# Performance work log

Measured on AMD Instinct MI355X. Metric: run time of the kernel, lower is better.

The kernel has to match this reference:

```python
import jax, jax.numpy as jnp
import numpy as np

L, D, H, S, V, B = 8, 512, 8, 64, 66, 256
DH = D // H
EPS = 1e-10  # module's LayerNorm eps, added to std (not var)


def layernorm(x, g, b):
    # torch.std_mean default: unbiased std (ddof=1)
    mean = jnp.mean(x, axis=-1, keepdims=True)
    std = jnp.std(x, axis=-1, ddof=1, keepdims=True)
    return (x - mean) / (std + EPS) * g + b


def setup_inputs() -> dict:
    key = jax.random.key(0)
    ks = iter(jax.random.split(key, 32))
    def n(shape, scale=0.02):
        return jax.random.normal(next(ks), shape, dtype=jnp.float32) * scale
    return {
        "input_ids": jax.random.randint(next(ks), (B, S), 0, V),
        "targets": jax.random.randint(next(ks), (B, S), 0, V),
        "tok_emb": n((V, D), 1.0),
        "pos_emb": n((S, D), 1.0),
        "Wq": n((L, D, H, DH)), "Wk": n((L, D, H, DH)), "Wv": n((L, D, H, DH)),
        "Wo": n((L, D, D)), "bo": jnp.zeros((L, D), jnp.float32),
        "W1": n((L, D, 4 * D)), "b1": jnp.zeros((L, 4 * D), jnp.float32),
        "W2": n((L, 4 * D, D)), "b2": jnp.zeros((L, D), jnp.float32),
        "ln1_g": jnp.ones((L, D), jnp.float32), "ln1_b": jnp.zeros((L, D), jnp.float32),
        "ln2_g": jnp.ones((L, D), jnp.float32), "ln2_b": jnp.zeros((L, D), jnp.float32),
        "lnf_g": jnp.ones((D,), jnp.float32), "lnf_b": jnp.zeros((D,), jnp.float32),
        "Wu": n((D, V)), "bu": jnp.zeros((V,), jnp.float32),
    }


def reference(input_ids, targets, tok_emb, pos_emb, Wq, Wk, Wv, Wo, bo,
              W1, b1, W2, b2, ln1_g, ln1_b, ln2_g, ln2_b, lnf_g, lnf_b, Wu, bu):
    x = tok_emb[input_ids] + pos_emb[None, :, :]  # [B,S,D]
    scale = 1.0 / jnp.sqrt(jnp.float32(D))        # module scales by 1/sqrt(d_model)
    mask = jnp.tril(jnp.ones((S, S), dtype=bool))
    for l in range(L):
        h = layernorm(x, ln1_g[l], ln1_b[l])
        q = jnp.einsum('bsd,dhe->bhse', h, Wq[l])
        k = jnp.einsum('bsd,dhe->bhse', h, Wk[l])
        v = jnp.einsum('bsd,dhe->bhse', h, Wv[l])
        scores = jnp.einsum('bhse,bhte->bhst', q, k) * scale
        scores = jnp.where(mask, scores, -jnp.inf)
        attn = jax.nn.softmax(scores, axis=-1)
        o = jnp.einsum('bhst,bhte->bhse', attn, v)
        o = o.transpose(0, 2, 1, 3).reshape(B, S, D)  # concat heads (head order preserved)
        x = x + o @ Wo[l] + bo[l]
        h2 = layernorm(x, ln2_g[l], ln2_b[l])
        hid = jax.nn.gelu(h2 @ W1[l] + b1[l], approximate=False)  # nn.GELU exact
        x = x + hid @ W2[l] + b2[l]
    x = layernorm(x, lnf_g, lnf_b)
    logits = x @ Wu + bu  # [B,S,V]
    logp = jax.nn.log_softmax(logits, axis=-1)
    loss = -jnp.mean(jnp.take_along_axis(logp, targets[..., None], axis=-1))
    return logits, loss
```

## Files before the change

### kernel.cpp

```cpp
#include <hip/hip_runtime.h>
#include <hip/hip_bf16.h>
#include <math.h>

#define D_MODEL 512
#define NHEAD   8
#define DHEAD   64
#define SEQ     64
#define BATCH   256
#define NLAYER  8
#define VOCAB   66
#define FFDIM   2048
#define NTOK    (BATCH * SEQ)

typedef __attribute__((ext_vector_type(8))) short short8;
typedef __attribute__((ext_vector_type(4))) float f32x4;

__device__ inline void async_copy16(const void* g, void* l) {
    __builtin_amdgcn_global_load_lds(
        (const __attribute__((address_space(1))) void*)g,
        (__attribute__((address_space(3))) void*)l,
        16, 0, 0);
}

__global__ __launch_bounds__(256) void transpose_conv(
        const float* __restrict__ W, __hip_bfloat16* __restrict__ Wt,
        int K, int M, size_t inLS, size_t outLS, int rowOff) {
    __shared__ float tile[32][33];
    int m0 = blockIdx.x * 32, k0 = blockIdx.y * 32;
    const float* Wl = W + blockIdx.z * inLS;
    __hip_bfloat16* Wtl = Wt + blockIdx.z * outLS;
    int t = threadIdx.x;
    #pragma unroll
    for (int p = 0; p < 4; p++) {
        int idx = t + p * 256;
        int kr = idx >> 5, mc = idx & 31;
        tile[kr][mc] = Wl[(size_t)(k0 + kr) * M + m0 + mc];
    }
    __syncthreads();
    #pragma unroll
    for (int p = 0; p < 4; p++) {
        int idx = t + p * 256;
        int mr = idx >> 5, kc = idx & 31;
        Wtl[(size_t)(rowOff + m0 + mr) * K + k0 + kc] = __float2bfloat16(tile[kc][mr]);
    }
}

__global__ __launch_bounds__(256) void conv_wu(
        const float* __restrict__ Wu, __hip_bfloat16* __restrict__ WuT) {
    int idx = blockIdx.x * 256 + threadIdx.x;
    int m = idx >> 9, k = idx & 511;
    WuT[idx] = __float2bfloat16(m < VOCAB ? Wu[(size_t)k * VOCAB + m] : 0.f);
}

__global__ void embed_kernel(const int* __restrict__ ids, const float* __restrict__ tok,
                             const float* __restrict__ pos, float* __restrict__ x) {
    int idx = blockIdx.x * 256 + threadIdx.x;
    int n = idx >> 9;
    int d = idx & 511;
    int s = n & (SEQ - 1);
    x[idx] = tok[ids[n] * D_MODEL + d] + pos[s * D_MODEL + d];
}

__global__ void ln_kernel(const float* __restrict__ x, const float* __restrict__ g,
                          const float* __restrict__ b, __hip_bfloat16* __restrict__ y) {
    int row = blockIdx.x;
    const float* xr = x + (size_t)row * D_MODEL;
    int t = threadIdx.x;
    float v0 = xr[t], v1 = xr[t + 256];
    float s = v0 + v1, ss = v0 * v0 + v1 * v1;
    #pragma unroll
    for (int o = 32; o >= 1; o >>= 1) {
        s  += __shfl_down(s, o);
        ss += __shfl_down(ss, o);
    }
    __shared__ float ws[4], wss[4];
    int wid = t >> 6, lane = t & 63;
    if (lane == 0) { ws[wid] = s; wss[wid] = ss; }
    __syncthreads();
    if (t == 0) {
        float S = ws[0] + ws[1] + ws[2] + ws[3];
        float SS = wss[0] + wss[1] + wss[2] + wss[3];
        float mean = S / (float)D_MODEL;
        float var = (SS - (float)D_MODEL * mean * mean) / (float)(D_MODEL - 1);
        var = fmaxf(var, 0.f);
        ws[0] = mean;
        wss[0] = sqrtf(var) + 1e-10f;
    }
    __syncthreads();
    float mean = ws[0], denom = wss[0];
    __hip_bfloat16* yr = y + (size_t)row * D_MODEL;
    yr[t]       = __float2bfloat16((v0 - mean) / denom * g[t]       + b[t]);
    yr[t + 256] = __float2bfloat16((v1 - mean) / denom * g[t + 256] + b[t + 256]);
}

template <int ACT, int OUTMODE>
__global__ __launch_bounds__(256) void mfma_gemm(
        const __hip_bfloat16* __restrict__ A, const __hip_bfloat16* __restrict__ Bt,
        const float* __restrict__ bias, const float* addsrc,
        void* Cout, int K, int M, int ldc, int mstore) {
    __shared__ __align__(16) short As[128 * 32];
    __shared__ __align__(16) short Bs[128 * 32];
    int tid = threadIdx.x;
    int lane = tid & 63, wave = tid >> 6;
    int row0 = blockIdx.y * 128, col0 = blockIdx.x * 128;
    int wr = (wave >> 1) * 64, wc = (wave & 1) * 64;
    int l15 = lane & 15, quad = lane >> 4;

    f32x4 acc[4][4] = {};

    int sr = tid >> 2;
    int scol = (tid & 3) * 8;
    const short* Ag = (const short*)A + (size_t)(row0 + sr) * K + scol;
    const short* Bg = (const short*)Bt + (size_t)(col0 + sr) * K + scol;
    short* Al = As + sr * 32 + scol;
    short* Bl = Bs + sr * 32 + scol;

    for (int k0 = 0; k0 < K; k0 += 32) {
        async_copy16(Ag + k0, Al);
        async_copy16(Ag + (size_t)64 * K + k0, Al + 64 * 32);
        async_copy16(Bg + k0, Bl);
        async_copy16(Bg + (size_t)64 * K + k0, Bl + 64 * 32);
        __syncthreads();
        short8 af[4], bf[4];
        #pragma unroll
        for (int i = 0; i < 4; i++)
            af[i] = *(const short8*)(As + (wr + i * 16 + l15) * 32 + quad * 8);
        #pragma unroll
        for (int j = 0; j < 4; j++)
            bf[j] = *(const short8*)(Bs + (wc + j * 16 + l15) * 32 + quad * 8);
        #pragma unroll
        for (int i = 0; i < 4; i++)
            #pragma unroll
            for (int j = 0; j < 4; j++)
                acc[i][j] = __builtin_amdgcn_mfma_f32_16x16x32_bf16(af[i], bf[j], acc[i][j], 0, 0, 0);
        __syncthreads();
    }

    #pragma unroll
    for (int j = 0; j < 4; j++) {
        int col = col0 + wc + j * 16 + l15;
        if (OUTMODE == 2 && col >= mstore) continue;
        float bv = bias ? bias[col] : 0.f;
        #pragma unroll
        for (int i = 0; i < 4; i++) {
            int rbase = row0 + wr + i * 16 + quad * 4;
            #pragma unroll
            for (int r = 0; r < 4; r++) {
                int row = rbase + r;
                float v = acc[i][j][r] + bv;
                if (OUTMODE == 1) v += addsrc[(size_t)row * M + col];
                if (ACT == 1) v = 0.5f * v * (1.f + erff(v * 0.70710678118654752f));
                if (OUTMODE == 0)
                    ((__hip_bfloat16*)Cout)[(size_t)row * M + col] = __float2bfloat16(v);
                else
                    ((float*)Cout)[(size_t)row * ldc + col] = v;
            }
        }
    }
}

#define PSTRIDE 72
__global__ __launch_bounds__(256) void attn_mfma(
        const __hip_bfloat16* __restrict__ QKV, __hip_bfloat16* __restrict__ O) {
    __shared__ __align__(16) short Vt[64 * PSTRIDE];
    __shared__ __align__(16) short P[64 * PSTRIDE];
    int bh = blockIdx.x;
    int b = bh >> 3, h = bh & 7;
    int t = threadIdx.x;
    int lane = t & 63, wave = t >> 6;
    int l15 = lane & 15, quad = lane >> 4;
    const float scale = 0.04419417382415922f;
    const short* base = (const short*)QKV + (size_t)(b * SEQ) * 1536 + h * DHEAD;

    {
        int j0 = (t >> 3) * 2;
        int c0 = (t & 7) * 8;
        const short* vrow = base + 1024 + (size_t)j0 * 1536 + c0;
        short8 va = *(const short8*)vrow;
        short8 vb = *(const short8*)(vrow + 1536);
        #pragma unroll
        for (int s = 0; s < 8; s++) {
            unsigned int packed = ((unsigned int)(unsigned short)vb[s] << 16) |
                                  (unsigned int)(unsigned short)va[s];
            *(unsigned int*)&Vt[(c0 + s) * PSTRIDE + j0] = packed;
        }
    }

    int r0 = wave * 16;
    short8 aq[2], bk[4][2];
    #pragma unroll
    for (int k = 0; k < 2; k++)
        aq[k] = *(const short8*)(base + (size_t)(r0 + l15) * 1536 + quad * 8 + 32 * k);
    #pragma unroll
    for (int j = 0; j < 4; j++)
        #pragma unroll
        for (int k = 0; k < 2; k++)
            bk[j][k] = *(const short8*)(base + 512 + (size_t)(j * 16 + l15) * 1536 + quad * 8 + 32 * k);

    f32x4 sc[4];
    #pragma unroll
    for (int j = 0; j < 4; j++) {
        f32x4 z = {};
        z = __builtin_amdgcn_mfma_f32_16x16x32_bf16(aq[0], bk[j][0], z, 0, 0, 0);
        sc[j] = __builtin_amdgcn_mfma_f32_16x16x32_bf16(aq[1], bk[j][1], z, 0, 0, 0);
    }

    float p[4][4];
    #pragma unroll
    for (int reg = 0; reg < 4; reg++) {
        int r = r0 + quad * 4 + reg;
        float m = -INFINITY;
        #pragma unroll
        for (int j = 0; j < 4; j++) {
            int c = j * 16 + l15;
            float s = (c <= r) ? sc[j][reg] * scale : -INFINITY;
            p[j][reg] = s;
            m = fmaxf(m, s);
        }
        #pragma unroll
        for (int o = 1; o < 16; o <<= 1) m = fmaxf(m, __shfl_xor(m, o));
        float sum = 0.f;
        #pragma unroll
        for (int j = 0; j < 4; j++) {
            float e = (p[j][reg] == -INFINITY) ? 0.f : expf(p[j][reg] - m);
            p[j][reg] = e;
            sum += e;
        }
        #pragma unroll
        for (int o = 1; o < 16; o <<= 1) sum += __shfl_xor(sum, o);
        float inv = 1.f / sum;
        #pragma unroll
        for (int j = 0; j < 4; j++) p[j][reg] *= inv;
    }

    #pragma unroll
    for (int j = 0; j < 4; j++)
        #pragma unroll
        for (int reg = 0; reg < 4; reg++) {
            int r = r0 + quad * 4 + reg;
            P[r * PSTRIDE + j * 16 + l15] =
                ((__hip_bfloat16_raw)__float2bfloat16(p[j][reg])).x;
        }

    __syncthreads();

    short8 ap[2];
    #pragma unroll
    for (int k = 0; k < 2; k++)
        ap[k] = *(const short8*)(P + (r0 + l15) * PSTRIDE + quad * 8 + 32 * k);
    #pragma unroll
    for (int jt = 0; jt < 4; jt++) {
        short8 bv0 = *(const short8*)(Vt + (jt * 16 + l15) * PSTRIDE + quad * 8);
        short8 bv1 = *(const short8*)(Vt + (jt * 16 + l15) * PSTRIDE + quad * 8 + 32);
        f32x4 o = {};
        o = __builtin_amdgcn_mfma_f32_16x16x32_bf16(ap[0], bv0, o, 0, 0, 0);
        o = __builtin_amdgcn_mfma_f32_16x16x32_bf16(ap[1], bv1, o, 0, 0, 0);
        #pragma unroll
        for (int reg = 0; reg < 4; reg++) {
            int r = r0 + quad * 4 + reg;
            int c = jt * 16 + l15;
            O[(size_t)(b * SEQ + r) * D_MODEL + h * DHEAD + c] = __float2bfloat16(o[reg]);
        }
    }
}

__global__ void zero_kernel(float* p) { if (threadIdx.x == 0) *p = 0.f; }

__global__ __launch_bounds__(256) void loss_kernel(
        const float* __restrict__ lg, const int* __restrict__ tgt,
        float* __restrict__ loss) {
    int row = blockIdx.x * 4 + (threadIdx.x >> 6);
    int l = threadIdx.x & 63;
    const float* lr = lg + (size_t)row * VOCAB;
    float a = lr[l];
    float bx = (l < VOCAB - 64) ? lr[64 + l] : -INFINITY;
    float m = fmaxf(a, bx);
    #pragma unroll
    for (int o = 32; o >= 1; o >>= 1) m = fmaxf(m, __shfl_xor(m, o));
    float s = expf(a - m) + ((l < VOCAB - 64) ? expf(bx - m) : 0.f);
    #pragma unroll
    for (int o = 32; o >= 1; o >>= 1) s += __shfl_xor(s, o);
    if (l == 0) {
        float lp = lr[tgt[row]] - m - logf(s);
        atomicAdd(loss, -lp / (float)NTOK);
    }
}

extern "C" void kernel_launch(void* const* d_in, const int* in_sizes, int n_in,
                              void* d_out, int out_size, void* d_ws, size_t ws_size,
                              hipStream_t stream) {
    const int*   input_ids = (const int*)  d_in[0];
    const int*   targets   = (const int*)  d_in[1];
    const float* tok_emb   = (const float*)d_in[2];
    const float* pos_emb   = (const float*)d_in[3];
    const float* Wq        = (const float*)d_in[4];
    const float* Wk        = (const float*)d_in[5];
    const float* Wv        = (const float*)d_in[6];
    const float* Wo        = (const float*)d_in[7];
    const float* bo        = (const float*)d_in[8];
    const float* W1        = (const float*)d_in[9];
    const float* b1        = (const float*)d_in[10];
    const float* W2        = (const float*)d_in[11];
    const float* b2        = (const float*)d_in[12];
    const float* ln1_g     = (const float*)d_in[13];
    const float* ln1_b     = (const float*)d_in[14];
    const float* ln2_g     = (const float*)d_in[15];
    const float* ln2_b     = (const float*)d_in[16];
    const float* lnf_g     = (const float*)d_in[17];
    const float* lnf_b     = (const float*)d_in[18];
    const float* Wu        = (const float*)d_in[19];
    const float* bu        = (const float*)d_in[20];

    float* out  = (float*)d_out;
    float* loss = out + (size_t)NTOK * VOCAB;

    const size_t ND = (size_t)NTOK * D_MODEL;
    float* x             = (float*)d_ws;
    __hip_bfloat16* h    = (__hip_bfloat16*)(x + ND);
    __hip_bfloat16* qkv  = h + ND;
    __hip_bfloat16* ob   = qkv + 3 * ND;
    __hip_bfloat16* hid  = qkv;
    __hip_bfloat16* wqkvT = ob + ND;
    __hip_bfloat16* woT   = wqkvT + (size_t)NLAYER * 1536 * 512;
    __hip_bfloat16* w1T   = woT + (size_t)NLAYER * 512 * 512;
    __hip_bfloat16* w2T   = w1T + (size_t)NLAYER * 2048 * 512;
    __hip_bfloat16* wuT   = w2T + (size_t)NLAYER * 2048 * 512;

    transpose_conv<<<dim3(16, 16, NLAYER), 256, 0, stream>>>(Wq, wqkvT, 512, 512,
        (size_t)512 * 512, (size_t)1536 * 512, 0);
    transpose_conv<<<dim3(16, 16, NLAYER), 256, 0, stream>>>(Wk, wqkvT, 512, 512,
        (size_t)512 * 512, (size_t)1536 * 512, 512);
    transpose_conv<<<dim3(16, 16, NLAYER), 256, 0, stream>>>(Wv, wqkvT, 512, 512,
        (size_t)512 * 512, (size_t)1536 * 512, 1024);
    transpose_conv<<<dim3(16, 16, NLAYER), 256, 0, stream>>>(Wo, woT, 512, 512,
        (size_t)512 * 512, (size_t)512 * 512, 0);
    transpose_conv<<<dim3(64, 16, NLAYER), 256, 0, stream>>>(W1, w1T, 512, 2048,
        (size_t)512 * 2048, (size_t)2048 * 512, 0);
    transpose_conv<<<dim3(16, 64, NLAYER), 256, 0, stream>>>(W2, w2T, 2048, 512,
        (size_t)2048 * 512, (size_t)512 * 2048, 0);
    conv_wu<<<(128 * 512) / 256, 256, 0, stream>>>(Wu, wuT);

    embed_kernel<<<(NTOK * D_MODEL) / 256, 256, 0, stream>>>(input_ids, tok_emb, pos_emb, x);

    for (int l = 0; l < NLAYER; l++) {
        ln_kernel<<<NTOK, 256, 0, stream>>>(x, ln1_g + l * D_MODEL, ln1_b + l * D_MODEL, h);
        mfma_gemm<0, 0><<<dim3(12, 128), 256, 0, stream>>>(
            h, wqkvT + (size_t)l * 1536 * 512, nullptr, nullptr, qkv, 512, 1536, 1536, 1536);
        attn_mfma<<<BATCH * NHEAD, 256, 0, stream>>>(qkv, ob);
        mfma_gemm<0, 1><<<dim3(4, 128), 256, 0, stream>>>(
            ob, woT + (size_t)l * 512 * 512, bo + l * D_MODEL, x, x, 512, 512, 512, 512);
        ln_kernel<<<NTOK, 256, 0, stream>>>(x, ln2_g + l * D_MODEL, ln2_b + l * D_MODEL, h);
        mfma_gemm<1, 0><<<dim3(16, 128), 256, 0, stream>>>(
            h, w1T + (size_t)l * 2048 * 512, b1 + l * FFDIM, nullptr, hid, 512, 2048, 2048, 2048);
        mfma_gemm<0, 1><<<dim3(4, 128), 256, 0, stream>>>(
            hid, w2T + (size_t)l * 2048 * 512, b2 + l * D_MODEL, x, x, 2048, 512, 512, 512);
    }

    ln_kernel<<<NTOK, 256, 0, stream>>>(x, lnf_g, lnf_b, h);
    mfma_gemm<0, 2><<<dim3(1, 128), 256, 0, stream>>>(
        h, wuT, bu, nullptr, out, 512, 128, VOCAB, VOCAB);
    zero_kernel<<<1, 64, 0, stream>>>(loss);
    loss_kernel<<<NTOK / 4, 256, 0, stream>>>(out, targets, loss);
}
```

Before: 2.508 ms.

## Use 32x32 MFMA in GEMM, wave-per-row LayerNorm, grid-stride loss reduction

```diff
diff --git a/kernel.cpp b/kernel.cpp
--- a/kernel.cpp
+++ b/kernel.cpp
@@ -14,6 +14,7 @@
 
 typedef __attribute__((ext_vector_type(8))) short short8;
 typedef __attribute__((ext_vector_type(4))) float f32x4;
+typedef __attribute__((ext_vector_type(16))) float f32x16;
 
 __device__ inline void async_copy16(const void* g, void* l) {
     __builtin_amdgcn_global_load_lds(
@@ -61,36 +62,36 @@
     x[idx] = tok[ids[n] * D_MODEL + d] + pos[s * D_MODEL + d];
 }
 
-__global__ void ln_kernel(const float* __restrict__ x, const float* __restrict__ g,
-                          const float* __restrict__ b, __hip_bfloat16* __restrict__ y) {
-    int row = blockIdx.x;
-    const float* xr = x + (size_t)row * D_MODEL;
-    int t = threadIdx.x;
-    float v0 = xr[t], v1 = xr[t + 256];
-    float s = v0 + v1, ss = v0 * v0 + v1 * v1;
-    #pragma unroll
-    for (int o = 32; o >= 1; o >>= 1) {
-        s  += __shfl_down(s, o);
-        ss += __shfl_down(ss, o);
-    }
-    __shared__ float ws[4], wss[4];
-    int wid = t >> 6, lane = t & 63;
-    if (lane == 0) { ws[wid] = s; wss[wid] = ss; }
-    __syncthreads();
-    if (t == 0) {
-        float S = ws[0] + ws[1] + ws[2] + ws[3];
-        float SS = wss[0] + wss[1] + wss[2] + wss[3];
-        float mean = S / (float)D_MODEL;
-        float var = (SS - (float)D_MODEL * mean * mean) / (float)(D_MODEL - 1);
-        var = fmaxf(var, 0.f);
-        ws[0] = mean;
-        wss[0] = sqrtf(var) + 1e-10f;
-    }
-    __syncthreads();
-    float mean = ws[0], denom = wss[0];
-    __hip_bfloat16* yr = y + (size_t)row * D_MODEL;
-    yr[t]       = __float2bfloat16((v0 - mean) / denom * g[t]       + b[t]);
-    yr[t + 256] = __float2bfloat16((v1 - mean) / denom * g[t + 256] + b[t + 256]);
+__global__ __launch_bounds__(256) void ln_kernel(
+        const float* __restrict__ x, const float* __restrict__ g,
+        const float* __restrict__ b, __hip_bfloat16* __restrict__ y) {
+    int row = blockIdx.x * 4 + (threadIdx.x >> 6);
+    int lane = threadIdx.x & 63;
+    const float* xr = x + (size_t)row * D_MODEL + lane * 8;
+    f32x4 v0 = *(const f32x4*)xr;
+    f32x4 v1 = *(const f32x4*)(xr + 4);
+    float s = 0.f, ss = 0.f;
+    #pragma unroll
+    for (int e = 0; e < 4; e++) { s += v0[e] + v1[e]; ss += v0[e] * v0[e] + v1[e] * v1[e]; }
+    #pragma unroll
+    for (int o = 1; o < 64; o <<= 1) {
+        s  += __shfl_xor(s, o);
+        ss += __shfl_xor(ss, o);
+    }
+    float mean = s / (float)D_MODEL;
+    float var = (ss - (float)D_MODEL * mean * mean) / (float)(D_MODEL - 1);
+    float denom = sqrtf(fmaxf(var, 0.f)) + 1e-10f;
+    f32x4 g0 = *(const f32x4*)(g + lane * 8);
+    f32x4 g1 = *(const f32x4*)(g + lane * 8 + 4);
+    f32x4 b0 = *(const f32x4*)(b + lane * 8);
+    f32x4 b1 = *(const f32x4*)(b + lane * 8 + 4);
+    short8 outv;
+    #pragma unroll
+    for (int e = 0; e < 4; e++) {
+        outv[e]     = ((__hip_bfloat16_raw)__float2bfloat16((v0[e] - mean) / denom * g0[e] + b0[e])).x;
+        outv[e + 4] = ((__hip_bfloat16_raw)__float2bfloat16((v1[e] - mean) / denom * g1[e] + b1[e])).x;
+    }
+    *(short8*)((short*)y + (size_t)row * D_MODEL + lane * 8) = outv;
 }
 
 template <int ACT, int OUTMODE>
@@ -104,9 +105,9 @@
     int lane = tid & 63, wave = tid >> 6;
     int row0 = blockIdx.y * 128, col0 = blockIdx.x * 128;
     int wr = (wave >> 1) * 64, wc = (wave & 1) * 64;
-    int l15 = lane & 15, quad = lane >> 4;
-
-    f32x4 acc[4][4] = {};
+    int l31 = lane & 31, h32 = lane >> 5;
+
+    f32x16 acc[2][2] = {};
 
     int sr = tid >> 2;
     int scol = (tid & 3) * 8;
@@ -121,32 +122,35 @@
         async_copy16(Bg + k0, Bl);
         async_copy16(Bg + (size_t)64 * K + k0, Bl + 64 * 32);
         __syncthreads();
-        short8 af[4], bf[4];
-        #pragma unroll
-        for (int i = 0; i < 4; i++)
-            af[i] = *(const short8*)(As + (wr + i * 16 + l15) * 32 + quad * 8);
-        #pragma unroll
-        for (int j = 0; j < 4; j++)
-            bf[j] = *(const short8*)(Bs + (wc + j * 16 + l15) * 32 + quad * 8);
-        #pragma unroll
-        for (int i = 0; i < 4; i++)
+        short8 af[2][2], bf[2][2];
+        #pragma unroll
+        for (int i = 0; i < 2; i++)
             #pragma unroll
-            for (int j = 0; j < 4; j++)
-                acc[i][j] = __builtin_amdgcn_mfma_f32_16x16x32_bf16(af[i], bf[j], acc[i][j], 0, 0, 0);
+            for (int kh = 0; kh < 2; kh++) {
+                af[i][kh] = *(const short8*)(As + (wr + i * 32 + l31) * 32 + kh * 16 + h32 * 8);
+                bf[i][kh] = *(const short8*)(Bs + (wc + i * 32 + l31) * 32 + kh * 16 + h32 * 8);
+            }
+        #pragma unroll
+        for (int i = 0; i < 2; i++)
+            #pragma unroll
+            for (int j = 0; j < 2; j++) {
+                acc[i][j] = __builtin_amdgcn_mfma_f32_32x32x16_bf16(af[i][0], bf[j][0], acc[i][j], 0, 0, 0);
+                acc[i][j] = __builtin_amdgcn_mfma_f32_32x32x16_bf16(af[i][1], bf[j][1], acc[i][j], 0, 0, 0);
+            }
         __syncthreads();
     }
 
     #pragma unroll
-    for (int j = 0; j < 4; j++) {
-        int col = col0 + wc + j * 16 + l15;
+    for (int j = 0; j < 2; j++) {
+        int col = col0 + wc + j * 32 + l31;
         if (OUTMODE == 2 && col >= mstore) continue;
         float bv = bias ? bias[col] : 0.f;
         #pragma unroll
-        for (int i = 0; i < 4; i++) {
-            int rbase = row0 + wr + i * 16 + quad * 4;
+        for (int i = 0; i < 2; i++) {
+            int rbase = row0 + wr + i * 32 + 4 * h32;
             #pragma unroll
-            for (int r = 0; r < 4; r++) {
-                int row = rbase + r;
+            for (int r = 0; r < 16; r++) {
+                int row = rbase + (r & 3) + 8 * (r >> 2);
                 float v = acc[i][j][r] + bv;
                 if (OUTMODE == 1) v += addsrc[(size_t)row * M + col];
                 if (ACT == 1) v = 0.5f * v * (1.f + erff(v * 0.70710678118654752f));
@@ -269,21 +273,22 @@
 __global__ __launch_bounds__(256) void loss_kernel(
         const float* __restrict__ lg, const int* __restrict__ tgt,
         float* __restrict__ loss) {
-    int row = blockIdx.x * 4 + (threadIdx.x >> 6);
+    int wave = threadIdx.x >> 6;
     int l = threadIdx.x & 63;
-    const float* lr = lg + (size_t)row * VOCAB;
-    float a = lr[l];
-    float bx = (l < VOCAB - 64) ? lr[64 + l] : -INFINITY;
-    float m = fmaxf(a, bx);
-    #pragma unroll
-    for (int o = 32; o >= 1; o >>= 1) m = fmaxf(m, __shfl_xor(m, o));
-    float s = expf(a - m) + ((l < VOCAB - 64) ? expf(bx - m) : 0.f);
-    #pragma unroll
-    for (int o = 32; o >= 1; o >>= 1) s += __shfl_xor(s, o);
-    if (l == 0) {
-        float lp = lr[tgt[row]] - m - logf(s);
-        atomicAdd(loss, -lp / (float)NTOK);
-    }
+    float local = 0.f;
+    for (int row = blockIdx.x * 4 + wave; row < NTOK; row += gridDim.x * 4) {
+        const float* lr = lg + (size_t)row * VOCAB;
+        float a = lr[l];
+        float bx = (l < VOCAB - 64) ? lr[64 + l] : -INFINITY;
+        float m = fmaxf(a, bx);
+        #pragma unroll
+        for (int o = 32; o >= 1; o >>= 1) m = fmaxf(m, __shfl_xor(m, o));
+        float s = expf(a - m) + ((l < VOCAB - 64) ? expf(bx - m) : 0.f);
+        #pragma unroll
+        for (int o = 32; o >= 1; o >>= 1) s += __shfl_xor(s, o);
+        if (l == 0) local += lr[tgt[row]] - m - logf(s);
+    }
+    if (l == 0) atomicAdd(loss, -local / (float)NTOK);
 }
 
 extern "C" void kernel_launch(void* const* d_in, const int* in_sizes, int n_in,
@@ -343,22 +348,22 @@
     embed_kernel<<<(NTOK * D_MODEL) / 256, 256, 0, stream>>>(input_ids, tok_emb, pos_emb, x);
 
     for (int l = 0; l < NLAYER; l++) {
-        ln_kernel<<<NTOK, 256, 0, stream>>>(x, ln1_g + l * D_MODEL, ln1_b + l * D_MODEL, h);
+        ln_kernel<<<NTOK / 4, 256, 0, stream>>>(x, ln1_g + l * D_MODEL, ln1_b + l * D_MODEL, h);
         mfma_gemm<0, 0><<<dim3(12, 128), 256, 0, stream>>>(
             h, wqkvT + (size_t)l * 1536 * 512, nullptr, nullptr, qkv, 512, 1536, 1536, 1536);
         attn_mfma<<<BATCH * NHEAD, 256, 0, stream>>>(qkv, ob);
         mfma_gemm<0, 1><<<dim3(4, 128), 256, 0, stream>>>(
             ob, woT + (size_t)l * 512 * 512, bo + l * D_MODEL, x, x, 512, 512, 512, 512);
-        ln_kernel<<<NTOK, 256, 0, stream>>>(x, ln2_g + l * D_MODEL, ln2_b + l * D_MODEL, h);
+        ln_kernel<<<NTOK / 4, 256, 0, stream>>>(x, ln2_g + l * D_MODEL, ln2_b + l * D_MODEL, h);
         mfma_gemm<1, 0><<<dim3(16, 128), 256, 0, stream>>>(
             h, w1T + (size_t)l * 2048 * 512, b1 + l * FFDIM, nullptr, hid, 512, 2048, 2048, 2048);
         mfma_gemm<0, 1><<<dim3(4, 128), 256, 0, stream>>>(
             hid, w2T + (size_t)l * 2048 * 512, b2 + l * D_MODEL, x, x, 2048, 512, 512, 512);
     }
 
-    ln_kernel<<<NTOK, 256, 0, stream>>>(x, lnf_g, lnf_b, h);
+    ln_kernel<<<NTOK / 4, 256, 0, stream>>>(x, lnf_g, lnf_b, h);
     mfma_gemm<0, 2><<<dim3(1, 128), 256, 0, stream>>>(
         h, wuT, bu, nullptr, out, 512, 128, VOCAB, VOCAB);
     zero_kernel<<<1, 64, 0, stream>>>(loss);
-    loss_kernel<<<NTOK / 4, 256, 0, stream>>>(out, targets, loss);
-}
+    loss_kernel<<<128, 256, 0, stream>>>(out, targets, loss);
+}
```

New measurement: 2.395 ms. 4.5% less time.
